# Kernel optimization log

Hardware: AMD Instinct MI355X
Metric: run time of the kernel (lower is better)

## Reference

```python
import jax, jax.numpy as jnp
import numpy as np

B, T, D = 4, 2048, 1024
H, KVH = 16, 4          # query heads, kv heads
HD = D // H             # head_dim = 64
R = 32                  # partial rope dims
ROPE_BASE = 10000.0
EPS = 1e-6


def rmsnorm(x, scale):
    # per-head RMSNorm over last dim, computed in fp32 like the torch code
    xf = x.astype(jnp.float32)
    norm = jax.lax.rsqrt(jnp.mean(xf * xf, axis=-1, keepdims=True) + EPS)
    return (xf * norm).astype(x.dtype) * scale


def apply_rope(x, cos, sin):
    # x: (B,T,H,HD); rotate first R dims, pass the rest through
    x_r, x_p = x[..., :R], x[..., R:]
    half = R // 2
    x1, x2 = x_r[..., :half], x_r[..., half:]
    rotated = jnp.concatenate([x1 * cos - x2 * sin, x1 * sin + x2 * cos], axis=-1)
    return jnp.concatenate([rotated, x_p], axis=-1)


def setup_inputs() -> dict:
    key = jax.random.key(0)
    ks = jax.random.split(key, 8)
    x = jax.random.normal(ks[0], (B, T, D), dtype=jnp.float32)
    # RoPE tables exactly as RotaryEmbedding.get_cos_sin
    inv_freq = 1.0 / (ROPE_BASE ** (jnp.arange(0, R, 2, dtype=jnp.float32) / R))
    t = jnp.arange(T, dtype=jnp.float32)
    freqs = jnp.outer(t, inv_freq)                      # (T, R/2)
    cos = jnp.cos(freqs)[None, :, None, :]              # (1,T,1,R/2)
    sin = jnp.sin(freqs)[None, :, None, :]
    s = 1.0 / np.sqrt(D)
    Wq = jax.random.normal(ks[1], (D, D), dtype=jnp.float32) * s
    Wk = jax.random.normal(ks[2], (KVH * HD, D), dtype=jnp.float32) * s
    Wv = jax.random.normal(ks[3], (KVH * HD, D), dtype=jnp.float32) * s
    Wo = jax.random.normal(ks[4], (D, D), dtype=jnp.float32) * s
    q_scale = jnp.ones((HD,), dtype=jnp.float32)
    k_scale = jnp.ones((HD,), dtype=jnp.float32)
    return {"x": x, "cos": cos, "sin": sin, "Wq": Wq, "Wk": Wk, "Wv": Wv,
            "Wo": Wo, "q_scale": q_scale, "k_scale": k_scale}


def reference(x, cos, sin, Wq, Wk, Wv, Wo, q_scale, k_scale):
    b, t, d = x.shape
    q = jnp.einsum('btd,ed->bte', x, Wq).reshape(b, t, H, HD)
    k = jnp.einsum('btd,ed->bte', x, Wk).reshape(b, t, KVH, HD)
    v = jnp.einsum('btd,ed->bte', x, Wv).reshape(b, t, KVH, HD)
    q = apply_rope(rmsnorm(q, q_scale), cos, sin)
    k = apply_rope(rmsnorm(k, k_scale), cos, sin)
    groups = H // KVH
    k = jnp.repeat(k, groups, axis=2)   # (b,t,H,HD), matches repeat_interleave dim=2
    v = jnp.repeat(v, groups, axis=2)
    q = q.transpose(0, 2, 1, 3)         # (b,H,t,HD)
    k = k.transpose(0, 2, 1, 3)
    v = v.transpose(0, 2, 1, 3)
    scores = jnp.einsum('bhqd,bhkd->bhqk', q, k) / np.sqrt(HD)
    causal = jnp.tril(jnp.ones((t, t), dtype=bool))
    scores = jnp.where(causal, scores, -jnp.inf)
    attn = jax.nn.softmax(scores, axis=-1)
    y = jnp.einsum('bhqk,bhkd->bhqd', attn, v)
    y = y.transpose(0, 2, 1, 3).reshape(b, t, d)
    return jnp.einsum('btd,ed->bte', y, Wo)
```

## Files before the change

### kernel.cpp

```cpp
#include <hip/hip_runtime.h>
#include <hip/hip_bf16.h>
#include <stdint.h>

typedef __attribute__((ext_vector_type(8)))  __bf16 bf16x8;
typedef __attribute__((ext_vector_type(4)))  float  f32x4;
typedef __attribute__((ext_vector_type(16))) float  f32x16;
typedef __hip_bfloat16 bf16_t;

#define T_SEQ 2048
#define D_MODEL 1024
#define N_HEADS 16
#define N_KV 4
#define HD 64
#define LDQKV 1536
#define KDIM 1024

__device__ inline void cvt16(const float4* __restrict__ g, int4* __restrict__ s) {
  float4 v0 = g[0], v1 = g[1], v2 = g[2], v3 = g[3];
  union { int4 i[2]; __hip_bfloat162 h[8]; } u;
  u.h[0] = __float22bfloat162_rn(make_float2(v0.x, v0.y));
  u.h[1] = __float22bfloat162_rn(make_float2(v0.z, v0.w));
  u.h[2] = __float22bfloat162_rn(make_float2(v1.x, v1.y));
  u.h[3] = __float22bfloat162_rn(make_float2(v1.z, v1.w));
  u.h[4] = __float22bfloat162_rn(make_float2(v2.x, v2.y));
  u.h[5] = __float22bfloat162_rn(make_float2(v2.z, v2.w));
  u.h[6] = __float22bfloat162_rn(make_float2(v3.x, v3.y));
  u.h[7] = __float22bfloat162_rn(make_float2(v3.z, v3.w));
  s[0] = u.i[0]; s[1] = u.i[1];
}

__device__ inline void storeC(bf16_t* p, float v) { *p = __float2bfloat16(v); }
__device__ inline void storeC(float* p, float v) { *p = v; }

__device__ inline void plswap(unsigned& a, unsigned& b) {
  asm volatile("v_permlane32_swap_b32 %0, %1" : "+v"(a), "+v"(b));
}

__device__ inline float fexp2(float x) {
  float r; asm("v_exp_f32 %0, %1" : "=v"(r) : "v"(x)); return r;
}
__device__ inline unsigned cvtpk(float lo, float hi) {
  unsigned r; asm("v_cvt_pk_bf16_f32 %0, %1, %2" : "=v"(r) : "v"(lo), "v"(hi));
  return r;
}

__device__ inline void gll16(const bf16_t* g, bf16_t* l) {
  __builtin_amdgcn_global_load_lds(
      (const __attribute__((address_space(1))) void*)g,
      (__attribute__((address_space(3))) void*)l, 16, 0, 0);
}

__global__ __launch_bounds__(256) void all_cvt(
    const float* __restrict__ x,
    const float* __restrict__ Wq, const float* __restrict__ Wk,
    const float* __restrict__ Wv, const float* __restrict__ Wo,
    bf16_t* __restrict__ xb, bf16_t* __restrict__ wqkvb,
    bf16_t* __restrict__ wob) {
  const int i = blockIdx.x * 256 + threadIdx.x;
  const float* s; bf16_t* d; int off;
  if (i < 524288)      { s = x;  d = xb;                   off = i; }
  else if (i < 589824) { s = Wq; d = wqkvb;                off = i - 524288; }
  else if (i < 606208) { s = Wk; d = wqkvb + 1024 * 1024;  off = i - 589824; }
  else if (i < 622592) { s = Wv; d = wqkvb + 1280 * 1024;  off = i - 606208; }
  else                 { s = Wo; d = wob;                  off = i - 622592; }
  cvt16((const float4*)s + off * 4, (int4*)d + off * 2);
}

template <int MODE, typename CT>
__global__ __launch_bounds__(256) void gemm_bb(
    const bf16_t* __restrict__ A, const bf16_t* __restrict__ W,
    CT* __restrict__ C, const int ldC,
    const float* __restrict__ cosb, const float* __restrict__ sinb,
    const float* __restrict__ qs, const float* __restrict__ ks,
    bf16_t* __restrict__ v_t)
{
  __shared__ bf16_t As[128 * 32];
  __shared__ bf16_t Bs[128 * 32];
  const int tid = threadIdx.x;
  const int lane = tid & 63;
  const int wv = tid >> 6;
  const int wr = wv >> 1, wc = wv & 1;
  const int m0 = blockIdx.y * 128;
  const int n0 = blockIdx.x * 128;

  const int srow = lane >> 2;
  const int scol = (lane & 3) * 8;
  const bf16_t* gA = A + (size_t)(m0 + 32 * wv + srow) * KDIM + scol;
  const bf16_t* gB = W + (size_t)(n0 + 32 * wv + srow) * KDIM + scol;
  bf16_t* lA = As + wv * 1024;
  bf16_t* lB = Bs + wv * 1024;

  f32x4 acc[4][4];
#pragma unroll
  for (int m = 0; m < 4; ++m)
#pragma unroll
    for (int n = 0; n < 4; ++n)
      acc[m][n] = {0.f, 0.f, 0.f, 0.f};

  const int fr = lane & 15;
  const int fq = lane >> 4;

  for (int k0 = 0; k0 < KDIM; k0 += 32) {
    gll16(gA + k0, lA);
    gll16(gA + 16 * KDIM + k0, lA + 512);
    gll16(gB + k0, lB);
    gll16(gB + 16 * KDIM + k0, lB + 512);
    __syncthreads();
    bf16x8 af[4], bfv[4];
#pragma unroll
    for (int m = 0; m < 4; ++m)
      af[m] = *(const bf16x8*)(&As[(wr * 64 + m * 16 + fr) * 32 + fq * 8]);
#pragma unroll
    for (int n = 0; n < 4; ++n)
      bfv[n] = *(const bf16x8*)(&Bs[(wc * 64 + n * 16 + fr) * 32 + fq * 8]);
#pragma unroll
    for (int m = 0; m < 4; ++m)
#pragma unroll
      for (int n = 0; n < 4; ++n)
        acc[m][n] = __builtin_amdgcn_mfma_f32_16x16x32_bf16(af[m], bfv[n],
                                                            acc[m][n], 0, 0, 0);
    __syncthreads();
  }

  if (MODE == 0 || n0 < 1280) {
    if (MODE == 1) {
      const float* stab = (n0 < 1024) ? qs : ks;
      float sc0 = stab[fr], sc1 = stab[16 + fr], sc2 = stab[32 + fr], sc3 = stab[48 + fr];
#pragma unroll
      for (int m = 0; m < 4; ++m)
#pragma unroll
        for (int r = 0; r < 4; ++r) {
          const int row = m0 + wr * 64 + m * 16 + fq * 4 + r;
          const int t = row & (T_SEQ - 1);
          float ss = acc[m][0][r] * acc[m][0][r] + acc[m][1][r] * acc[m][1][r]
                   + acc[m][2][r] * acc[m][2][r] + acc[m][3][r] * acc[m][3][r];
          ss += __shfl_xor(ss, 1);
          ss += __shfl_xor(ss, 2);
          ss += __shfl_xor(ss, 4);
          ss += __shfl_xor(ss, 8);
          const float nrm = rsqrtf(ss * (1.f / 64.f) + 1e-6f);
          const float v0 = acc[m][0][r] * nrm * sc0;
          const float v1 = acc[m][1][r] * nrm * sc1;
          const float v2 = acc[m][2][r] * nrm * sc2;
          const float v3 = acc[m][3][r] * nrm * sc3;
          const float c = cosb[t * 16 + fr];
          const float s = sinb[t * 16 + fr];
          const float r0 = v0 * c - v1 * s;
          const float r1 = v0 * s + v1 * c;
          bf16_t* p = (bf16_t*)C + (size_t)row * ldC + n0 + wc * 64 + fr;
          p[0]  = __float2bfloat16(r0);
          p[16] = __float2bfloat16(r1);
          p[32] = __float2bfloat16(v2);
          p[48] = __float2bfloat16(v3);
        }
    } else {
#pragma unroll
      for (int m = 0; m < 4; ++m)
#pragma unroll
        for (int n = 0; n < 4; ++n)
#pragma unroll
          for (int r = 0; r < 4; ++r) {
            const int row = wr * 64 + m * 16 + fq * 4 + r;
            const int col = wc * 64 + n * 16 + fr;
            storeC(&C[(size_t)(m0 + row) * ldC + n0 + col], acc[m][n][r]);
          }
    }
  } else {
#pragma unroll
    for (int m = 0; m < 4; ++m) {
      const int row0 = m0 + wr * 64 + m * 16 + fq * 4;
      const int b = row0 >> 11, t0 = row0 & (T_SEQ - 1);
#pragma unroll
      for (int n = 0; n < 4; ++n) {
        const int vcol = n0 - 1280 + wc * 64 + n * 16 + fr;
        const int g = b * 4 + (vcol >> 6);
        const int d = vcol & 63;
        uint2 pk2;
        pk2.x = cvtpk(acc[m][n][0], acc[m][n][1]);
        pk2.y = cvtpk(acc[m][n][2], acc[m][n][3]);
        *(uint2*)(v_t + ((size_t)g * HD + d) * T_SEQ + t0) = pk2;
      }
    }
  }
}

__global__ __launch_bounds__(512) void attn(
    const bf16_t* __restrict__ qkv, const bf16_t* __restrict__ v_t,
    bf16_t* __restrict__ y)
{
  __shared__ int4 lds[4096];
  const int tid  = threadIdx.x;
  const int lane = tid & 63;
  const int w    = tid >> 6;
  const int spair= w >> 1;
  const int h    = w & 1;
  const int ql   = lane & 31;
  const int hi   = lane >> 5;
  const int id   = (int)blockIdx.x;
  const int low3 = id & 7;
  const int rest = id >> 3;
  const int gsel = rest & 1;
  const int hh   = (rest >> 1) & 3;
  const int p    = rest >> 3;
  const int g16  = low3 + 8 * gsel;
  const int b    = g16 >> 2, kvh = g16 & 3;
  const int hd   = kvh * 4 + hh;
  const int sA   = 4 * p + spair;
  const float SCALE_LOG2 = 0.125f * 1.44269504089f;

  const int sid = tid & 255;
  const int u2  = tid >> 8;
  const int kr = sid >> 3, kslot = sid & 7;
  const int vd = sid >> 2, vslot = sid & 3;
  const bf16_t* gK = qkv + (size_t)(b * T_SEQ + kr + u2 * 32) * LDQKV + 1024 + kvh * HD + kslot * 8;
  const bf16_t* gV = v_t + (size_t)((b * N_KV + kvh) * HD + vd) * T_SEQ + vslot * 8 + u2 * 32;
  const int wK0 = u2 * 256 + kr * 8 + (kslot ^ (kr & 7));
  const int wV0 = 1024 + u2 * 256 + vd * 4 + (vslot ^ ((vd >> 1) & 3));

  int kridx[4];
#pragma unroll
  for (int c = 0; c < 4; ++c)
    kridx[c] = ql * 8 + ((2 * c + hi) ^ (ql & 7));
  const int vsw = (ql >> 1) & 3;
  const int v0r = ql * 4 + (hi ^ vsw);
  const int v1r = ql * 4 + ((2 + hi) ^ vsw);
  const int v2r = (ql + 32) * 4 + (hi ^ vsw);
  const int v3r = (ql + 32) * 4 + ((2 + hi) ^ vsw);

  union ob { unsigned uu[4]; bf16x8 v; } onesf;
#pragma unroll
  for (int i = 0; i < 4; ++i) onesf.uu[i] = 0x3F803F80u;

  f32x16 zro;
#pragma unroll
  for (int i = 0; i < 16; ++i) zro[i] = 0.f;

  float* lf = (float*)lds;
  int buf = 0;
#pragma unroll
  for (int pi = 0; pi < 2; ++pi) {
    const int s = pi ? (63 - sA) : sA;
    const int q_glob = s * 32 + ql;
    const int nt = s + 1;
    const int nR = pi ? (16 - p) : (p + 1);

    const bf16_t* Qrow = qkv + (size_t)(b * T_SEQ + q_glob) * LDQKV + hd * HD + hi * 8;
    bf16x8 qfrag[4];
#pragma unroll
    for (int c = 0; c < 4; ++c) {
      bf16x8 raw = *(const bf16x8*)(Qrow + c * 16);
      bf16x8 sc;
#pragma unroll
      for (int j = 0; j < 8; ++j)
        sc[j] = (__bf16)((float)raw[j] * SCALE_LOG2);
      qfrag[c] = sc;
    }

    f32x16 acc0, acc1, accL;
#pragma unroll
    for (int i = 0; i < 16; ++i) { acc0[i] = 0.f; acc1[i] = 0.f; accL[i] = 0.f; }
    float m_run = -1e30f;

    {
      int4 a0 = *(const int4*)gK;
      int4 a1 = *(const int4*)(gK + (size_t)64 * LDQKV);
      int4 a2 = *(const int4*)gV;
      int4 a3 = *(const int4*)(gV + 64);
      const int nb = buf * 2048;
      lds[nb + wK0] = a0; lds[nb + wK0 + 512] = a1;
      lds[nb + wV0] = a2; lds[nb + wV0 + 512] = a3;
    }
    __syncthreads();

    for (int r = 0; r < nR; ++r) {
      int4 kA0, kA1, vA0, vA1;
      const bool more = (r + 1 < nR);
      if (more) {
        const bf16_t* k1 = gK + (size_t)(r + 1) * 128 * LDQKV;
        const bf16_t* v1 = gV + (r + 1) * 128;
        kA0 = *(const int4*)k1;
        kA1 = *(const int4*)(k1 + (size_t)64 * LDQKV);
        vA0 = *(const int4*)v1;
        vA1 = *(const int4*)(v1 + 64);
      }

#pragma unroll
      for (int uu = 0; uu < 2; ++uu) {
        const int t = 4 * r + 2 * h + uu;
        if (t < nt) {
          const int k0 = t << 5;
          const bool masked = (t == nt - 1);
          const int su = 2 * h + uu;
          const int kbase = buf * 2048 + su * 256;
          const int vbase = buf * 2048 + 1024 + su * 256;

          bf16x8 kf0 = *(const bf16x8*)&lds[kbase + kridx[0]];
          bf16x8 kf1 = *(const bf16x8*)&lds[kbase + kridx[1]];
          bf16x8 kf2 = *(const bf16x8*)&lds[kbase + kridx[2]];
          bf16x8 kf3 = *(const bf16x8*)&lds[kbase + kridx[3]];

          __builtin_amdgcn_s_setprio(1);
          f32x16 st = __builtin_amdgcn_mfma_f32_32x32x16_bf16(kf0, qfrag[0], zro, 0, 0, 0);
          st = __builtin_amdgcn_mfma_f32_32x32x16_bf16(kf1, qfrag[1], st, 0, 0, 0);
          st = __builtin_amdgcn_mfma_f32_32x32x16_bf16(kf2, qfrag[2], st, 0, 0, 0);
          st = __builtin_amdgcn_mfma_f32_32x32x16_bf16(kf3, qfrag[3], st, 0, 0, 0);
          __builtin_amdgcn_s_setprio(0);

          if (masked) {
#pragma unroll
            for (int rr = 0; rr < 16; ++rr) {
              const int kg = k0 + (rr & 3) + 8 * (rr >> 2) + 4 * hi;
              if (kg > q_glob) st[rr] = -1e30f;
            }
          }
          float m01 = fmaxf(fmaxf(st[0], st[1]), st[2]);
          float m02 = fmaxf(fmaxf(st[3], st[4]), st[5]);
          float m03 = fmaxf(fmaxf(st[6], st[7]), st[8]);
          float m04 = fmaxf(fmaxf(st[9], st[10]), st[11]);
          float m05 = fmaxf(fmaxf(st[12], st[13]), st[14]);
          float m06 = fmaxf(fmaxf(m01, m02), m03);
          float m07 = fmaxf(fmaxf(m04, m05), st[15]);
          const float bmax = fmaxf(m06, m07);
          if (__any(bmax > m_run + 8.f)) {
            const float rmax = fmaxf(bmax, __shfl_xor(bmax, 32));
            const float mnew = fmaxf(m_run, rmax);
            const float corr = fexp2(m_run - mnew);
#pragma unroll
            for (int i = 0; i < 16; ++i) { acc0[i] *= corr; acc1[i] *= corr; }
            accL[0] *= corr;
            m_run = mnew;
          }
          float pp[16];
#pragma unroll
          for (int rr = 0; rr < 16; ++rr) pp[rr] = fexp2(st[rr] - m_run);

          unsigned wp[8];
#pragma unroll
          for (int i = 0; i < 8; ++i) wp[i] = cvtpk(pp[2 * i], pp[2 * i + 1]);
          plswap(wp[0], wp[2]); plswap(wp[1], wp[3]);
          plswap(wp[4], wp[6]); plswap(wp[5], wp[7]);
          union fu { unsigned uu2[4]; bf16x8 v; };
          fu f1, f2;
          f1.uu2[0] = wp[0]; f1.uu2[1] = wp[1]; f1.uu2[2] = wp[2]; f1.uu2[3] = wp[3];
          f2.uu2[0] = wp[4]; f2.uu2[1] = wp[5]; f2.uu2[2] = wp[6]; f2.uu2[3] = wp[7];

          bf16x8 vf0 = *(const bf16x8*)&lds[vbase + v0r];
          bf16x8 vf1 = *(const bf16x8*)&lds[vbase + v1r];
          bf16x8 vf2 = *(const bf16x8*)&lds[vbase + v2r];
          bf16x8 vf3 = *(const bf16x8*)&lds[vbase + v3r];

          __builtin_amdgcn_s_setprio(1);
          acc0 = __builtin_amdgcn_mfma_f32_32x32x16_bf16(vf0, f1.v, acc0, 0, 0, 0);
          acc0 = __builtin_amdgcn_mfma_f32_32x32x16_bf16(vf1, f2.v, acc0, 0, 0, 0);
          acc1 = __builtin_amdgcn_mfma_f32_32x32x16_bf16(vf2, f1.v, acc1, 0, 0, 0);
          acc1 = __builtin_amdgcn_mfma_f32_32x32x16_bf16(vf3, f2.v, acc1, 0, 0, 0);
          accL = __builtin_amdgcn_mfma_f32_32x32x16_bf16(onesf.v, f1.v, accL, 0, 0, 0);
          accL = __builtin_amdgcn_mfma_f32_32x32x16_bf16(onesf.v, f2.v, accL, 0, 0, 0);
          __builtin_amdgcn_s_setprio(0);
        }
      }

      if (more) {
        const int nb = (buf ^ 1) * 2048;
        lds[nb + wK0] = kA0; lds[nb + wK0 + 512] = kA1;
        lds[nb + wV0] = vA0; lds[nb + wV0 + 512] = vA1;
      }
      __syncthreads();
      buf ^= 1;
    }

    float cA = 1.f, cB = 0.f, l_mrg = 0.f;
    if (h == 1) {
      const int fb = spair * 1216 + lane * 19;
#pragma unroll
      for (int i = 0; i < 16; ++i) lf[fb + i] = acc0[i];
      lf[fb + 16] = m_run;
      lf[fb + 17] = accL[0];
    }
    __syncthreads();
    if (h == 0) {
      const int fb = spair * 1216 + lane * 19;
      const float mB = lf[fb + 16], lB = lf[fb + 17];
      const float mM = fmaxf(m_run, mB);
      cA = fexp2(m_run - mM);
      cB = fexp2(mB - mM);
      l_mrg = accL[0] * cA + lB * cB;
#pragma unroll
      for (int i = 0; i < 16; ++i) acc0[i] = acc0[i] * cA + lf[fb + i] * cB;
    }
    __syncthreads();
    if (h == 1) {
      const int fb2 = spair * 1088 + lane * 17;
#pragma unroll
      for (int i = 0; i < 16; ++i) lf[fb2 + i] = acc1[i];
    }
    __syncthreads();
    if (h == 0) {
      const int fb2 = spair * 1088 + lane * 17;
#pragma unroll
      for (int i = 0; i < 16; ++i) acc1[i] = acc1[i] * cA + lf[fb2 + i] * cB;
      const float inv = 1.f / l_mrg;
      bf16_t* yrow = y + (size_t)(b * T_SEQ + q_glob) * D_MODEL + hd * HD;
#pragma unroll
      for (int gg = 0; gg < 4; ++gg) {
        uint2 o0, o1;
        o0.x = cvtpk(acc0[4 * gg + 0] * inv, acc0[4 * gg + 1] * inv);
        o0.y = cvtpk(acc0[4 * gg + 2] * inv, acc0[4 * gg + 3] * inv);
        o1.x = cvtpk(acc1[4 * gg + 0] * inv, acc1[4 * gg + 1] * inv);
        o1.y = cvtpk(acc1[4 * gg + 2] * inv, acc1[4 * gg + 3] * inv);
        *(uint2*)(yrow + 8 * gg + 4 * hi)      = o0;
        *(uint2*)(yrow + 32 + 8 * gg + 4 * hi) = o1;
      }
    }
    __syncthreads();
  }
}

extern "C" void kernel_launch(void* const* d_in, const int* in_sizes, int n_in,
                              void* d_out, int out_size, void* d_ws,
                              size_t ws_size, hipStream_t stream) {
  const float* x    = (const float*)d_in[0];
  const float* cosb = (const float*)d_in[1];
  const float* sinb = (const float*)d_in[2];
  const float* Wq   = (const float*)d_in[3];
  const float* Wk   = (const float*)d_in[4];
  const float* Wv   = (const float*)d_in[5];
  const float* Wo   = (const float*)d_in[6];
  const float* qs   = (const float*)d_in[7];
  const float* ks   = (const float*)d_in[8];
  float* out = (float*)d_out;

  char* ws = (char*)d_ws;
  bf16_t* qkv   = (bf16_t*)ws;
  bf16_t* v_t   = (bf16_t*)(ws + 25165824);
  bf16_t* y     = (bf16_t*)(ws + 29360128);
  bf16_t* xb    = y;
  bf16_t* wqkvb = (bf16_t*)(ws + 46137344);
  bf16_t* wob   = (bf16_t*)(ws + 49283072);

  all_cvt<<<dim3(2688), 256, 0, stream>>>(x, Wq, Wk, Wv, Wo, xb, wqkvb, wob);

  gemm_bb<1, bf16_t><<<dim3(12, 64), 256, 0, stream>>>(
      xb, wqkvb, qkv, LDQKV, cosb, sinb, qs, ks, v_t);
  attn<<<dim3(512), 512, 0, stream>>>(qkv, v_t, y);
  gemm_bb<0, float><<<dim3(8, 64), 256, 0, stream>>>(
      y, wob, out, D_MODEL, nullptr, nullptr, nullptr, nullptr, nullptr);
}
```

Before: 158.8 us.

## Use direct global-to-LDS loads and process two key tiles per softmax step

Replaces the register-staged K/V prefetch (global load to registers, then an LDS store after compute) with gll16 direct global-to-LDS loads. Each wave now fetches one whole K or V slot with a new swizzled address mapping. The inner loop is restructured to compute the scores for both 32-key tiles a wave owns before a single combined max/rescale, then issue all the PV MFMAs together. This removes the VGPR staging and LDS write instructions, halves the online-softmax rescale checks, and gives the MFMA pipe longer independent chains. The cost is more live registers, and the changed swizzle has to match the existing read indices.

```diff
diff --git a/kernel.cpp b/kernel.cpp
--- a/kernel.cpp
+++ b/kernel.cpp
@@ -208,14 +208,25 @@
   const int sA   = 4 * p + spair;
   const float SCALE_LOG2 = 0.125f * 1.44269504089f;
 
-  const int sid = tid & 255;
-  const int u2  = tid >> 8;
-  const int kr = sid >> 3, kslot = sid & 7;
-  const int vd = sid >> 2, vslot = sid & 3;
-  const bf16_t* gK = qkv + (size_t)(b * T_SEQ + kr + u2 * 32) * LDQKV + 1024 + kvh * HD + kslot * 8;
-  const bf16_t* gV = v_t + (size_t)((b * N_KV + kvh) * HD + vd) * T_SEQ + vslot * 8 + u2 * 32;
-  const int wK0 = u2 * 256 + kr * 8 + (kslot ^ (kr & 7));
-  const int wV0 = 1024 + u2 * 256 + vd * 4 + (vslot ^ ((vd >> 1) & 3));
+  const bool isK = (w < 4);
+  const int su  = isK ? w : (w - 4);
+  const bf16_t* gsrc0;
+  size_t strideJ, strideR;
+  if (isK) {
+    const int row = su * 32 + (lane >> 3);
+    const int col = ((lane & 7) ^ (lane >> 3)) * 8;
+    gsrc0 = qkv + (size_t)(b * T_SEQ + row) * LDQKV + 1024 + kvh * HD + col;
+    strideJ = (size_t)8 * LDQKV;
+    strideR = (size_t)128 * LDQKV;
+  } else {
+    const int row = lane >> 2;
+    const int col = ((lane & 3) ^ ((lane >> 3) & 3)) * 8 + su * 32;
+    gsrc0 = v_t + (size_t)((b * N_KV + kvh) * HD + row) * T_SEQ + col;
+    strideJ = (size_t)16 * T_SEQ;
+    strideR = 128;
+  }
+  const int ldsSlotBase = w * 256;
+  const int ldsOff = isK ? ldsSlotBase : (1024 + su * 256);
 
   int kridx[4];
 #pragma unroll
@@ -261,110 +272,140 @@
     for (int i = 0; i < 16; ++i) { acc0[i] = 0.f; acc1[i] = 0.f; accL[i] = 0.f; }
     float m_run = -1e30f;
 
+    const bf16_t* gsrc = gsrc0;
     {
-      int4 a0 = *(const int4*)gK;
-      int4 a1 = *(const int4*)(gK + (size_t)64 * LDQKV);
-      int4 a2 = *(const int4*)gV;
-      int4 a3 = *(const int4*)(gV + 64);
-      const int nb = buf * 2048;
-      lds[nb + wK0] = a0; lds[nb + wK0 + 512] = a1;
-      lds[nb + wV0] = a2; lds[nb + wV0 + 512] = a3;
-    }
+      bf16_t* lb = (bf16_t*)&lds[buf * 2048 + ldsOff];
+#pragma unroll
+      for (int j = 0; j < 4; ++j)
+        gll16(gsrc + j * strideJ, lb + j * 512);
+    }
+    gsrc += strideR;
     __syncthreads();
 
     for (int r = 0; r < nR; ++r) {
-      int4 kA0, kA1, vA0, vA1;
       const bool more = (r + 1 < nR);
       if (more) {
-        const bf16_t* k1 = gK + (size_t)(r + 1) * 128 * LDQKV;
-        const bf16_t* v1 = gV + (r + 1) * 128;
-        kA0 = *(const int4*)k1;
-        kA1 = *(const int4*)(k1 + (size_t)64 * LDQKV);
-        vA0 = *(const int4*)v1;
-        vA1 = *(const int4*)(v1 + 64);
+        bf16_t* lb = (bf16_t*)&lds[(buf ^ 1) * 2048 + ldsOff];
+#pragma unroll
+        for (int j = 0; j < 4; ++j)
+          gll16(gsrc + j * strideJ, lb + j * 512);
+        gsrc += strideR;
       }
 
-#pragma unroll
-      for (int uu = 0; uu < 2; ++uu) {
-        const int t = 4 * r + 2 * h + uu;
-        if (t < nt) {
-          const int k0 = t << 5;
-          const bool masked = (t == nt - 1);
-          const int su = 2 * h + uu;
-          const int kbase = buf * 2048 + su * 256;
-          const int vbase = buf * 2048 + 1024 + su * 256;
-
-          bf16x8 kf0 = *(const bf16x8*)&lds[kbase + kridx[0]];
-          bf16x8 kf1 = *(const bf16x8*)&lds[kbase + kridx[1]];
-          bf16x8 kf2 = *(const bf16x8*)&lds[kbase + kridx[2]];
-          bf16x8 kf3 = *(const bf16x8*)&lds[kbase + kridx[3]];
-
-          __builtin_amdgcn_s_setprio(1);
-          f32x16 st = __builtin_amdgcn_mfma_f32_32x32x16_bf16(kf0, qfrag[0], zro, 0, 0, 0);
-          st = __builtin_amdgcn_mfma_f32_32x32x16_bf16(kf1, qfrag[1], st, 0, 0, 0);
-          st = __builtin_amdgcn_mfma_f32_32x32x16_bf16(kf2, qfrag[2], st, 0, 0, 0);
-          st = __builtin_amdgcn_mfma_f32_32x32x16_bf16(kf3, qfrag[3], st, 0, 0, 0);
-          __builtin_amdgcn_s_setprio(0);
-
-          if (masked) {
-#pragma unroll
-            for (int rr = 0; rr < 16; ++rr) {
-              const int kg = k0 + (rr & 3) + 8 * (rr >> 2) + 4 * hi;
-              if (kg > q_glob) st[rr] = -1e30f;
-            }
+      const int t0 = 4 * r + 2 * h;
+      const int t1 = t0 + 1;
+      if (t0 < nt) {
+        const bool act1 = (t1 < nt);
+        const int kb0 = buf * 2048 + (2 * h) * 256;
+        const int kb1 = kb0 + 256;
+        const int vb0 = buf * 2048 + 1024 + (2 * h) * 256;
+        const int vb1 = vb0 + 256;
+
+        bf16x8 ka0 = *(const bf16x8*)&lds[kb0 + kridx[0]];
+        bf16x8 ka1 = *(const bf16x8*)&lds[kb0 + kridx[1]];
+        bf16x8 ka2 = *(const bf16x8*)&lds[kb0 + kridx[2]];
+        bf16x8 ka3 = *(const bf16x8*)&lds[kb0 + kridx[3]];
+        bf16x8 kb0f = *(const bf16x8*)&lds[kb1 + kridx[0]];
+        bf16x8 kb1f = *(const bf16x8*)&lds[kb1 + kridx[1]];
+        bf16x8 kb2f = *(const bf16x8*)&lds[kb1 + kridx[2]];
+        bf16x8 kb3f = *(const bf16x8*)&lds[kb1 + kridx[3]];
+
+        __builtin_amdgcn_s_setprio(1);
+        f32x16 st0 = __builtin_amdgcn_mfma_f32_32x32x16_bf16(ka0, qfrag[0], zro, 0, 0, 0);
+        st0 = __builtin_amdgcn_mfma_f32_32x32x16_bf16(ka1, qfrag[1], st0, 0, 0, 0);
+        st0 = __builtin_amdgcn_mfma_f32_32x32x16_bf16(ka2, qfrag[2], st0, 0, 0, 0);
+        st0 = __builtin_amdgcn_mfma_f32_32x32x16_bf16(ka3, qfrag[3], st0, 0, 0, 0);
+        f32x16 st1 = __builtin_amdgcn_mfma_f32_32x32x16_bf16(kb0f, qfrag[0], zro, 0, 0, 0);
+        st1 = __builtin_amdgcn_mfma_f32_32x32x16_bf16(kb1f, qfrag[1], st1, 0, 0, 0);
+        st1 = __builtin_amdgcn_mfma_f32_32x32x16_bf16(kb2f, qfrag[2], st1, 0, 0, 0);
+        st1 = __builtin_amdgcn_mfma_f32_32x32x16_bf16(kb3f, qfrag[3], st1, 0, 0, 0);
+        __builtin_amdgcn_s_setprio(0);
+
+        if (t0 == nt - 1) {
+#pragma unroll
+          for (int rr = 0; rr < 16; ++rr) {
+            const int kg = (t0 << 5) + (rr & 3) + 8 * (rr >> 2) + 4 * hi;
+            if (kg > q_glob) st0[rr] = -1e30f;
           }
-          float m01 = fmaxf(fmaxf(st[0], st[1]), st[2]);
-          float m02 = fmaxf(fmaxf(st[3], st[4]), st[5]);
-          float m03 = fmaxf(fmaxf(st[6], st[7]), st[8]);
-          float m04 = fmaxf(fmaxf(st[9], st[10]), st[11]);
-          float m05 = fmaxf(fmaxf(st[12], st[13]), st[14]);
-          float m06 = fmaxf(fmaxf(m01, m02), m03);
-          float m07 = fmaxf(fmaxf(m04, m05), st[15]);
-          const float bmax = fmaxf(m06, m07);
-          if (__any(bmax > m_run + 8.f)) {
-            const float rmax = fmaxf(bmax, __shfl_xor(bmax, 32));
-            const float mnew = fmaxf(m_run, rmax);
-            const float corr = fexp2(m_run - mnew);
-#pragma unroll
-            for (int i = 0; i < 16; ++i) { acc0[i] *= corr; acc1[i] *= corr; }
-            accL[0] *= corr;
-            m_run = mnew;
+        }
+        if (!act1) {
+#pragma unroll
+          for (int rr = 0; rr < 16; ++rr) st1[rr] = -1e30f;
+        } else if (t1 == nt - 1) {
+#pragma unroll
+          for (int rr = 0; rr < 16; ++rr) {
+            const int kg = (t1 << 5) + (rr & 3) + 8 * (rr >> 2) + 4 * hi;
+            if (kg > q_glob) st1[rr] = -1e30f;
           }
-          float pp[16];
-#pragma unroll
-          for (int rr = 0; rr < 16; ++rr) pp[rr] = fexp2(st[rr] - m_run);
-
-          unsigned wp[8];
-#pragma unroll
-          for (int i = 0; i < 8; ++i) wp[i] = cvtpk(pp[2 * i], pp[2 * i + 1]);
-          plswap(wp[0], wp[2]); plswap(wp[1], wp[3]);
-          plswap(wp[4], wp[6]); plswap(wp[5], wp[7]);
-          union fu { unsigned uu2[4]; bf16x8 v; };
-          fu f1, f2;
-          f1.uu2[0] = wp[0]; f1.uu2[1] = wp[1]; f1.uu2[2] = wp[2]; f1.uu2[3] = wp[3];
-          f2.uu2[0] = wp[4]; f2.uu2[1] = wp[5]; f2.uu2[2] = wp[6]; f2.uu2[3] = wp[7];
-
-          bf16x8 vf0 = *(const bf16x8*)&lds[vbase + v0r];
-          bf16x8 vf1 = *(const bf16x8*)&lds[vbase + v1r];
-          bf16x8 vf2 = *(const bf16x8*)&lds[vbase + v2r];
-          bf16x8 vf3 = *(const bf16x8*)&lds[vbase + v3r];
-
-          __builtin_amdgcn_s_setprio(1);
-          acc0 = __builtin_amdgcn_mfma_f32_32x32x16_bf16(vf0, f1.v, acc0, 0, 0, 0);
-          acc0 = __builtin_amdgcn_mfma_f32_32x32x16_bf16(vf1, f2.v, acc0, 0, 0, 0);
-          acc1 = __builtin_amdgcn_mfma_f32_32x32x16_bf16(vf2, f1.v, acc1, 0, 0, 0);
-          acc1 = __builtin_amdgcn_mfma_f32_32x32x16_bf16(vf3, f2.v, acc1, 0, 0, 0);
-          accL = __builtin_amdgcn_mfma_f32_32x32x16_bf16(onesf.v, f1.v, accL, 0, 0, 0);
-          accL = __builtin_amdgcn_mfma_f32_32x32x16_bf16(onesf.v, f2.v, accL, 0, 0, 0);
-          __builtin_amdgcn_s_setprio(0);
         }
+
+        float ma = fmaxf(fmaxf(fmaxf(st0[0], st0[1]), fmaxf(st0[2], st0[3])),
+                         fmaxf(fmaxf(st0[4], st0[5]), fmaxf(st0[6], st0[7])));
+        ma = fmaxf(ma,
+             fmaxf(fmaxf(fmaxf(st0[8], st0[9]), fmaxf(st0[10], st0[11])),
+                   fmaxf(fmaxf(st0[12], st0[13]), fmaxf(st0[14], st0[15]))));
+        float mb = fmaxf(fmaxf(fmaxf(st1[0], st1[1]), fmaxf(st1[2], st1[3])),
+                         fmaxf(fmaxf(st1[4], st1[5]), fmaxf(st1[6], st1[7])));
+        mb = fmaxf(mb,
+             fmaxf(fmaxf(fmaxf(st1[8], st1[9]), fmaxf(st1[10], st1[11])),
+                   fmaxf(fmaxf(st1[12], st1[13]), fmaxf(st1[14], st1[15]))));
+        const float bmax = fmaxf(ma, mb);
+        if (__any(bmax > m_run + 8.f)) {
+          const float rmax = fmaxf(bmax, __shfl_xor(bmax, 32));
+          const float mnew = fmaxf(m_run, rmax);
+          const float corr = fexp2(m_run - mnew);
+#pragma unroll
+          for (int i = 0; i < 16; ++i) { acc0[i] *= corr; acc1[i] *= corr; }
+          accL[0] *= corr;
+          m_run = mnew;
+        }
+        float p0[16], p1[16];
+#pragma unroll
+        for (int rr = 0; rr < 16; ++rr) p0[rr] = fexp2(st0[rr] - m_run);
+#pragma unroll
+        for (int rr = 0; rr < 16; ++rr) p1[rr] = fexp2(st1[rr] - m_run);
+
+        unsigned wa[8], wb[8];
+#pragma unroll
+        for (int i = 0; i < 8; ++i) wa[i] = cvtpk(p0[2 * i], p0[2 * i + 1]);
+        plswap(wa[0], wa[2]); plswap(wa[1], wa[3]);
+        plswap(wa[4], wa[6]); plswap(wa[5], wa[7]);
+#pragma unroll
+        for (int i = 0; i < 8; ++i) wb[i] = cvtpk(p1[2 * i], p1[2 * i + 1]);
+        plswap(wb[0], wb[2]); plswap(wb[1], wb[3]);
+        plswap(wb[4], wb[6]); plswap(wb[5], wb[7]);
+        union fu { unsigned uu2[4]; bf16x8 v; };
+        fu fa1, fa2, fb1, fb2;
+        fa1.uu2[0] = wa[0]; fa1.uu2[1] = wa[1]; fa1.uu2[2] = wa[2]; fa1.uu2[3] = wa[3];
+        fa2.uu2[0] = wa[4]; fa2.uu2[1] = wa[5]; fa2.uu2[2] = wa[6]; fa2.uu2[3] = wa[7];
+        fb1.uu2[0] = wb[0]; fb1.uu2[1] = wb[1]; fb1.uu2[2] = wb[2]; fb1.uu2[3] = wb[3];
+        fb2.uu2[0] = wb[4]; fb2.uu2[1] = wb[5]; fb2.uu2[2] = wb[6]; fb2.uu2[3] = wb[7];
+
+        bf16x8 va0 = *(const bf16x8*)&lds[vb0 + v0r];
+        bf16x8 va1 = *(const bf16x8*)&lds[vb0 + v1r];
+        bf16x8 va2 = *(const bf16x8*)&lds[vb0 + v2r];
+        bf16x8 va3 = *(const bf16x8*)&lds[vb0 + v3r];
+        bf16x8 vb0f = *(const bf16x8*)&lds[vb1 + v0r];
+        bf16x8 vb1f = *(const bf16x8*)&lds[vb1 + v1r];
+        bf16x8 vb2f = *(const bf16x8*)&lds[vb1 + v2r];
+        bf16x8 vb3f = *(const bf16x8*)&lds[vb1 + v3r];
+
+        __builtin_amdgcn_s_setprio(1);
+        acc0 = __builtin_amdgcn_mfma_f32_32x32x16_bf16(va0, fa1.v, acc0, 0, 0, 0);
+        acc0 = __builtin_amdgcn_mfma_f32_32x32x16_bf16(va1, fa2.v, acc0, 0, 0, 0);
+        acc1 = __builtin_amdgcn_mfma_f32_32x32x16_bf16(va2, fa1.v, acc1, 0, 0, 0);
+        acc1 = __builtin_amdgcn_mfma_f32_32x32x16_bf16(va3, fa2.v, acc1, 0, 0, 0);
+        acc0 = __builtin_amdgcn_mfma_f32_32x32x16_bf16(vb0f, fb1.v, acc0, 0, 0, 0);
+        acc0 = __builtin_amdgcn_mfma_f32_32x32x16_bf16(vb1f, fb2.v, acc0, 0, 0, 0);
+        acc1 = __builtin_amdgcn_mfma_f32_32x32x16_bf16(vb2f, fb1.v, acc1, 0, 0, 0);
+        acc1 = __builtin_amdgcn_mfma_f32_32x32x16_bf16(vb3f, fb2.v, acc1, 0, 0, 0);
+        accL = __builtin_amdgcn_mfma_f32_32x32x16_bf16(onesf.v, fa1.v, accL, 0, 0, 0);
+        accL = __builtin_amdgcn_mfma_f32_32x32x16_bf16(onesf.v, fa2.v, accL, 0, 0, 0);
+        accL = __builtin_amdgcn_mfma_f32_32x32x16_bf16(onesf.v, fb1.v, accL, 0, 0, 0);
+        accL = __builtin_amdgcn_mfma_f32_32x32x16_bf16(onesf.v, fb2.v, accL, 0, 0, 0);
+        __builtin_amdgcn_s_setprio(0);
       }
 
-      if (more) {
-        const int nb = (buf ^ 1) * 2048;
-        lds[nb + wK0] = kA0; lds[nb + wK0 + 512] = kA1;
-        lds[nb + wV0] = vA0; lds[nb + wV0 + 512] = vA1;
-      }
       __syncthreads();
       buf ^= 1;
     }
```

Result: slower. 163.8 us (+3.1%).
